# Kernel tuning notes

Hardware: AMD Instinct MI355X
Metric: run time of the kernel (lower is better)

Reference implementation:

```python
import jax, jax.numpy as jnp
import numpy as np

B, CD, E, H, K, L, NB = 262144, 2, 64, 128, 32, 6, 2
TB = 6.0
MIN_BIN = 1e-3      # nflows DEFAULT_MIN_BIN_WIDTH / HEIGHT
MIN_DERIV = 1e-3    # nflows DEFAULT_MIN_DERIVATIVE
P = 3 * K - 1       # spline params per feature


def _rq_spline(y, uw, uh, ud):
    """Unconstrained rational-quadratic spline (linear tails), forward pass.
    y: [B]; uw, uh: [B,K]; ud: [B,K-1]. Returns (z [B], logabsdet [B])."""
    inside = (y >= -TB) & (y <= TB)
    const = float(np.log(np.exp(1.0 - MIN_DERIV) - 1.0))
    ud = jnp.pad(ud, ((0, 0), (1, 1)), constant_values=const)  # boundary deriv -> 1
    w = jax.nn.softmax(uw, axis=-1)
    w = MIN_BIN + (1.0 - MIN_BIN * K) * w
    cw = jnp.pad(jnp.cumsum(w, -1), ((0, 0), (1, 0)))
    cw = (2.0 * TB) * cw - TB
    cw = cw.at[:, 0].set(-TB).at[:, -1].set(TB)
    w = cw[:, 1:] - cw[:, :-1]
    hgt = jax.nn.softmax(uh, axis=-1)
    hgt = MIN_BIN + (1.0 - MIN_BIN * K) * hgt
    ch = jnp.pad(jnp.cumsum(hgt, -1), ((0, 0), (1, 0)))
    ch = (2.0 * TB) * ch - TB
    ch = ch.at[:, 0].set(-TB).at[:, -1].set(TB)
    hgt = ch[:, 1:] - ch[:, :-1]
    d = MIN_DERIV + jax.nn.softplus(ud)                       # [B,K+1]
    yc = jnp.clip(y, -TB, TB)
    locs = cw.at[:, -1].add(1e-6)                             # nflows searchsorted eps
    idx = jnp.clip(jnp.sum((yc[:, None] >= locs).astype(jnp.int32), -1) - 1, 0, K - 1)
    g = lambda a, i: jnp.take_along_axis(a, i[:, None], axis=1)[:, 0]
    cw_k, w_k = g(cw, idx), g(w, idx)
    ch_k, h_k = g(ch, idx), g(hgt, idx)
    d_k, d_k1 = g(d, idx), g(d, idx + 1)
    s_k = h_k / w_k
    th = (yc - cw_k) / w_k
    th1m = th * (1.0 - th)
    num = h_k * (s_k * th * th + d_k * th1m)
    den = s_k + (d_k + d_k1 - 2.0 * s_k) * th1m
    out = ch_k + num / den
    dnum = s_k * s_k * (d_k1 * th * th + 2.0 * s_k * th1m + d_k * (1.0 - th) ** 2)
    lad = jnp.log(dnum) - 2.0 * jnp.log(den)
    return jnp.where(inside, out, y), jnp.where(inside, lad, 0.0)


def setup_inputs() -> dict:
    key = jax.random.key(0)
    ks = iter(jax.random.split(key, 32))
    w = lambda shape, fan: jax.random.normal(next(ks), shape, jnp.float32) / np.sqrt(fan)
    inp = {
        "y": jax.random.normal(next(ks), (B, 1), jnp.float32),
        "context": jax.random.normal(next(ks), (B, CD), jnp.float32),
        "eW1": w((CD, E), CD), "eb1": jnp.zeros((E,), jnp.float32),
        "eW2": w((E, E), E),   "eb2": jnp.zeros((E,), jnp.float32),
        "eW3": w((E, E), E),   "eb3": jnp.zeros((E,), jnp.float32),
        # per-layer MADE conditioner (input->hidden weight is masked to 0 for features=1)
        "init_b": w((L, H), 1.0),
        "ctx_W": w((L, E, H), E), "ctx_b": jnp.zeros((L, H), jnp.float32),
        "blk_W1": w((L, NB, H, H), H), "blk_b1": jnp.zeros((L, NB, H), jnp.float32),
        "blk_W2": w((L, NB, H, H), H), "blk_b2": jnp.zeros((L, NB, H), jnp.float32),
        "blk_Wc": w((L, NB, E, H), E), "blk_bc": jnp.zeros((L, NB, H), jnp.float32),
        "out_W": w((L, H, P), H), "out_b": jnp.zeros((L, P), jnp.float32),
    }
    return inp


def reference(y, context, eW1, eb1, eW2, eb2, eW3, eb3, init_b, ctx_W, ctx_b,
              blk_W1, blk_b1, blk_W2, blk_b2, blk_Wc, blk_bc, out_W, out_b):
    emb = jax.nn.elu(context @ eW1 + eb1)
    emb = jax.nn.elu(emb @ eW2 + eb2)
    emb = jax.nn.elu(emb @ eW3 + eb3)            # [B,E]
    z = y[:, 0]
    total_lad = jnp.zeros_like(z)
    scale = np.sqrt(H).astype(np.float32)        # nflows divides widths/heights by sqrt(hidden)
    for l in range(L):
        h = init_b[l] + emb @ ctx_W[l] + ctx_b[l]
        for j in range(NB):                       # masked residual blocks (fully open for features=1)
            t = jax.nn.elu(h) @ blk_W1[l, j] + blk_b1[l, j]
            t = jax.nn.elu(t) @ blk_W2[l, j] + blk_b2[l, j]
            gate = jax.nn.sigmoid(emb @ blk_Wc[l, j] + blk_bc[l, j])  # GLU with context
            h = h + t * gate
        p = h @ out_W[l] + out_b[l]               # [B, 3K-1]
        z, lad = _rq_spline(z, p[:, :K] / scale, p[:, K:2 * K] / scale, p[:, 2 * K:])
        total_lad = total_lad + lad
    log_prob = -0.5 * z * z - 0.5 * np.float32(np.log(2.0 * np.pi)) + total_lad
    return log_prob
```

## Files before the change

kernel.cpp:

```cpp
#include <hip/hip_runtime.h>
#include <math.h>

typedef _Float16 hfrag  __attribute__((ext_vector_type(8)));
typedef _Float16 hpack  __attribute__((ext_vector_type(4)));
typedef float    accf   __attribute__((ext_vector_type(16)));

constexpr float cTB = 6.0f;
constexpr float cMB = 0.001f;
constexpr float cMD = 0.001f;

constexpr int SH = 136;
constexpr int SE = 72;
constexpr int SP = 100;

__device__ __forceinline__ float eluf(float x)  { return x > 0.f ? x : __expf(x) - 1.f; }
__device__ __forceinline__ float sigmf(float x) { return 1.f / (1.f + __expf(-x)); }
__device__ __forceinline__ float softplusf_(float x) { return x > 20.f ? x : log1pf(__expf(x)); }

__global__ void prep_frag(const float* __restrict__ src, _Float16* __restrict__ dst,
                          int K, int F, int Fpad, int total) {
  int idx = blockIdx.x * 256 + threadIdx.x;
  if (idx >= total) return;
  const int j    = idx & 7;
  const int lane = (idx >> 3) & 63;
  const int rest = idx >> 9;
  const int csteps = K >> 4;
  const int cstep  = rest % csteps;
  const int rest2  = rest / csteps;
  const int fslices = Fpad >> 5;
  const int fs = rest2 % fslices;
  const int n  = rest2 / fslices;
  const int f  = fs * 32 + (lane & 31);
  const int k  = cstep * 16 + ((lane >> 5) << 3) + j;
  float v = (f < F) ? src[((size_t)n * K + k) * F + f] : 0.f;
  dst[idx] = (_Float16)v;
}

__global__ void prep_bias(const float* __restrict__ gib, const float* __restrict__ gcb,
                          const float* __restrict__ gob, float* __restrict__ cb,
                          float* __restrict__ ob) {
  int i = blockIdx.x * 256 + threadIdx.x;
  if (i < 768) cb[i] = gib[i] + gcb[i];
  if (i < 576) {
    int l = i / 96, f = i % 96;
    ob[i] = (f < 95) ? gob[l * 95 + f] : 0.f;
  }
}

#define GEMM2(WBASE, BPTR, BSTRIDE, KDIM, A0, A1)                              \
  _Pragma("unroll")                                                            \
  for (int c = 0; c < (KDIM); c += 16) {                                       \
    hfrag av = *(const hfrag*)((WBASE) + (c << 5) + lane8);                    \
    hfrag b0 = *(const hfrag*)((BPTR) + col * (BSTRIDE) + c + q8);             \
    hfrag b1 = *(const hfrag*)((BPTR) + (32 + col) * (BSTRIDE) + c + q8);      \
    A0 = __builtin_amdgcn_mfma_f32_32x32x16_f16(av, b0, A0, 0, 0, 0);          \
    A1 = __builtin_amdgcn_mfma_f32_32x32x16_f16(av, b1, A1, 0, 0, 0);          \
  }

__global__ __launch_bounds__(256, 4) void nsf_mfma(
    const float* __restrict__ gy,   const float* __restrict__ gctx,
    const float* __restrict__ eW1,  const float* __restrict__ eb1,
    const float* __restrict__ eb2,  const float* __restrict__ eb3,
    const float* __restrict__ cbias, const float* __restrict__ bb1,
    const float* __restrict__ bb2,  const float* __restrict__ bbc,
    const float* __restrict__ obias,
    const _Float16* __restrict__ wE2T, const _Float16* __restrict__ wE3T,
    const _Float16* __restrict__ wCtxT, const _Float16* __restrict__ wW1T,
    const _Float16* __restrict__ wW2T,  const _Float16* __restrict__ wWcT,
    const _Float16* __restrict__ wOutT, float* __restrict__ gout)
{
  __shared__ _Float16 sA[64 * SH];
  __shared__ _Float16 sE[64 * SE];
  __shared__ _Float16 sP[64 * SP];

  const int tid  = threadIdx.x;
  const int wid  = tid >> 6;
  const int lane = tid & 63;
  const int col  = lane & 31;
  const int q    = lane >> 5;
  const int q8   = q * 8;
  const int q4   = q * 4;
  const int f0   = wid * 32;
  const int m0   = blockIdx.x * 64;
  const int lane8 = lane * 8;

  {
    const int m  = tid & 63;
    const int eg = tid >> 6;
    const float2 c2 = *(const float2*)&gctx[(size_t)(m0 + m) * 2];
    #pragma unroll
    for (int j = 0; j < 16; ++j) {
      const int e = eg * 16 + j;
      sE[m * SE + e] = (_Float16)eluf(c2.x * eW1[e] + c2.y * eW1[64 + e] + eb1[e]);
    }
  }
  __syncthreads();
  {
    const int ft = wid & 1, nt = wid >> 1;
    accf a = {};
    const _Float16* wr = wE2T + ft * 2048;
    #pragma unroll
    for (int c = 0; c < 64; c += 16) {
      hfrag av = *(const hfrag*)(wr + (c << 5) + lane8);
      hfrag bv = *(const hfrag*)(&sE[(nt * 32 + col) * SE + c + q8]);
      a = __builtin_amdgcn_mfma_f32_32x32x16_f16(av, bv, a, 0, 0, 0);
    }
    const int mrow = nt * 32 + col;
    __syncthreads();
    #pragma unroll
    for (int g = 0; g < 4; ++g) {
      const int e = 32 * ft + 8 * g + q4;
      const float4 b = *(const float4*)&eb2[e];
      hpack pk;
      #pragma unroll
      for (int r = 0; r < 4; ++r) pk[r] = (_Float16)eluf(a[4 * g + r] + (&b.x)[r]);
      *(hpack*)&sA[mrow * SE + e] = pk;
    }
  }
  __syncthreads();
  {
    const int ft = wid & 1, nt = wid >> 1;
    accf a = {};
    const _Float16* wr = wE3T + ft * 2048;
    #pragma unroll
    for (int c = 0; c < 64; c += 16) {
      hfrag av = *(const hfrag*)(wr + (c << 5) + lane8);
      hfrag bv = *(const hfrag*)(&sA[(nt * 32 + col) * SE + c + q8]);
      a = __builtin_amdgcn_mfma_f32_32x32x16_f16(av, bv, a, 0, 0, 0);
    }
    const int mrow = nt * 32 + col;
    #pragma unroll
    for (int g = 0; g < 4; ++g) {
      const int e = 32 * ft + 8 * g + q4;
      const float4 b = *(const float4*)&eb3[e];
      hpack pk;
      #pragma unroll
      for (int r = 0; r < 4; ++r) pk[r] = (_Float16)eluf(a[4 * g + r] + (&b.x)[r]);
      *(hpack*)&sE[mrow * SE + e] = pk;
    }
  }
  __syncthreads();

  float z = 0.f, lad = 0.f;
  if (tid < 64) z = gy[m0 + tid];

  accf h0, h1;

  #pragma unroll 1
  for (int l = 0; l < 6; ++l) {
    {
      accf a0 = {}, a1 = {};
      const _Float16* wr = wCtxT + (size_t)l * 8192 + wid * 2048;
      GEMM2(wr, sE, SE, 64, a0, a1)
      #pragma unroll
      for (int nt = 0; nt < 2; ++nt) {
        accf& A = nt ? a1 : a0;
        accf& H = nt ? h1 : h0;
        const int mrow = nt * 32 + col;
        #pragma unroll
        for (int g = 0; g < 4; ++g) {
          const int f = f0 + 8 * g + q4;
          const float4 bi = *(const float4*)&cbias[l * 128 + f];
          hpack pk;
          #pragma unroll
          for (int r = 0; r < 4; ++r) {
            float hv = A[4 * g + r] + (&bi.x)[r];
            H[4 * g + r] = hv;
            pk[r] = (_Float16)eluf(hv);
          }
          *(hpack*)&sA[mrow * SH + f] = pk;
        }
      }
    }
    __syncthreads();

    #pragma unroll 1
    for (int jb = 0; jb < 2; ++jb) {
      const int wi = l * 2 + jb;
      {
        accf a0 = {}, a1 = {};
        const _Float16* wr = wW1T + (size_t)wi * 16384 + wid * 4096;
        GEMM2(wr, sA, SH, 128, a0, a1)
        __syncthreads();
        #pragma unroll
        for (int nt = 0; nt < 2; ++nt) {
          accf& A = nt ? a1 : a0;
          const int mrow = nt * 32 + col;
          #pragma unroll
          for (int g = 0; g < 4; ++g) {
            const int f = f0 + 8 * g + q4;
            const float4 bv = *(const float4*)&bb1[wi * 128 + f];
            hpack pk;
            #pragma unroll
            for (int r = 0; r < 4; ++r) pk[r] = (_Float16)eluf(A[4 * g + r] + (&bv.x)[r]);
            *(hpack*)&sA[mrow * SH + f] = pk;
          }
        }
      }
      __syncthreads();
      {
        hpack gpk[2][4];
        {
          accf g0 = {}, g1 = {};
          const _Float16* wrc = wWcT + (size_t)wi * 8192 + wid * 2048;
          GEMM2(wrc, sE, SE, 64, g0, g1)
          #pragma unroll
          for (int nt = 0; nt < 2; ++nt) {
            accf& AG = nt ? g1 : g0;
            #pragma unroll
            for (int g = 0; g < 4; ++g) {
              const int f = f0 + 8 * g + q4;
              const float4 bcv = *(const float4*)&bbc[wi * 128 + f];
              #pragma unroll
              for (int r = 0; r < 4; ++r)
                gpk[nt][g][r] = (_Float16)sigmf(AG[4 * g + r] + (&bcv.x)[r]);
            }
          }
        }
        __builtin_amdgcn_sched_barrier(0);
        accf a0 = {}, a1 = {};
        const _Float16* wr2 = wW2T + (size_t)wi * 16384 + wid * 4096;
        GEMM2(wr2, sA, SH, 128, a0, a1)
        __syncthreads();
        const bool last = (jb == 1);
        #pragma unroll
        for (int nt = 0; nt < 2; ++nt) {
          accf& A2 = nt ? a1 : a0;
          accf& H  = nt ? h1 : h0;
          const int mrow = nt * 32 + col;
          #pragma unroll
          for (int g = 0; g < 4; ++g) {
            const int f = f0 + 8 * g + q4;
            const float4 b2v = *(const float4*)&bb2[wi * 128 + f];
            hpack pk;
            #pragma unroll
            for (int r = 0; r < 4; ++r) {
              const float hv = H[4 * g + r] + (A2[4 * g + r] + (&b2v.x)[r]) * (float)gpk[nt][g][r];
              H[4 * g + r] = hv;
              pk[r] = (_Float16)(last ? hv : eluf(hv));
            }
            *(hpack*)&sA[mrow * SH + f] = pk;
          }
        }
      }
      __syncthreads();
    }

    if (wid < 3) {
      accf o0 = {}, o1 = {};
      const _Float16* wr = wOutT + (size_t)l * 12288 + wid * 4096;
      GEMM2(wr, sA, SH, 128, o0, o1)
      #pragma unroll
      for (int nt = 0; nt < 2; ++nt) {
        accf& A = nt ? o1 : o0;
        const int mrow = nt * 32 + col;
        #pragma unroll
        for (int g = 0; g < 4; ++g) {
          const int f = f0 + 8 * g + q4;
          const float4 ov = *(const float4*)&obias[l * 96 + f];
          hpack pk;
          #pragma unroll
          for (int r = 0; r < 4; ++r) pk[r] = (_Float16)(A[4 * g + r] + (&ov.x)[r]);
          *(hpack*)&sP[mrow * SP + f] = pk;
        }
      }
    }
    __syncthreads();

    if (tid < 64) {
      const float invS = 0.08838834764831845f;
      const _Float16* pmv = &sP[tid * SP];
      auto pm = [&](int i) -> float { return (float)pmv[i]; };
      float mw = pm(0), mh = pm(32);
      #pragma unroll
      for (int i = 1; i < 32; ++i) {
        mw = fmaxf(mw, pm(i));
        mh = fmaxf(mh, pm(32 + i));
      }
      float sw = 0.f, sh = 0.f;
      #pragma unroll
      for (int i = 0; i < 32; ++i) {
        sw += __expf((pm(i) - mw) * invS);
        sh += __expf((pm(32 + i) - mh) * invS);
      }
      const float cw_scale = (1.0f - cMB * 32.f) / sw;
      const float ch_scale = (1.0f - cMB * 32.f) / sh;
      const float yc = fminf(fmaxf(z, -cTB), cTB);

      int idx = 0;
      float cum = 0.f, cw_k = -cTB, cw_k1 = cTB;
      bool take = true;
      #pragma unroll
      for (int i = 1; i <= 32; ++i) {
        float cwi;
        if (i < 32) {
          cum += cMB + __expf((pm(i - 1) - mw) * invS) * cw_scale;
          cwi = 2.f * cTB * cum - cTB;
        } else {
          cwi = cTB;
        }
        if (take) { cw_k1 = cwi; take = false; }
        if (i < 32 && yc >= cwi) { idx = i; cw_k = cwi; take = true; }
      }

      cum = 0.f;
      float ch_k = -cTB, ch_k1 = cTB;
      #pragma unroll
      for (int i = 1; i < 32; ++i) {
        cum += cMB + __expf((pm(32 + i - 1) - mh) * invS) * ch_scale;
        const float chi = 2.f * cTB * cum - cTB;
        if (i == idx) ch_k = chi;
        if (i == idx + 1) ch_k1 = chi;
      }

      const float w_k = cw_k1 - cw_k;
      const float h_k = ch_k1 - ch_k;
      const float d_k  = (idx == 0)  ? 1.f : cMD + softplusf_(pm(64 + idx - 1));
      const float d_k1 = (idx == 31) ? 1.f : cMD + softplusf_(pm(64 + idx));

      const float s_k  = h_k / w_k;
      const float th   = (yc - cw_k) / w_k;
      const float th1m = th * (1.f - th);
      const float numv = h_k * (s_k * th * th + d_k * th1m);
      const float denv = s_k + (d_k + d_k1 - 2.f * s_k) * th1m;
      const float outv = ch_k + numv / denv;
      const float omt  = 1.f - th;
      const float dnum = s_k * s_k * (d_k1 * th * th + 2.f * s_k * th1m + d_k * omt * omt);
      const float ladv = __logf(dnum) - 2.f * __logf(denv);
      const bool inside = (z >= -cTB) && (z <= cTB);
      if (inside) { z = outv; lad += ladv; }
    }
  }

  if (tid < 64) {
    gout[m0 + tid] = -0.5f * z * z - 0.9189385332046727f + lad;
  }
}

extern "C" void kernel_launch(void* const* d_in, const int* in_sizes, int n_in,
                              void* d_out, int out_size, void* d_ws, size_t ws_size,
                              hipStream_t stream) {
  const float* gy   = (const float*)d_in[0];
  const float* gctx = (const float*)d_in[1];
  const float* eW1  = (const float*)d_in[2];
  const float* eb1  = (const float*)d_in[3];
  const float* eW2  = (const float*)d_in[4];
  const float* eb2  = (const float*)d_in[5];
  const float* eW3  = (const float*)d_in[6];
  const float* eb3  = (const float*)d_in[7];
  const float* gib  = (const float*)d_in[8];
  const float* gcW  = (const float*)d_in[9];
  const float* gcb  = (const float*)d_in[10];
  const float* bW1  = (const float*)d_in[11];
  const float* bb1  = (const float*)d_in[12];
  const float* bW2  = (const float*)d_in[13];
  const float* bb2  = (const float*)d_in[14];
  const float* bWc  = (const float*)d_in[15];
  const float* bbc  = (const float*)d_in[16];
  const float* goW  = (const float*)d_in[17];
  const float* gob  = (const float*)d_in[18];

  _Float16* ws    = (_Float16*)d_ws;
  _Float16* wE2T  = ws;
  _Float16* wE3T  = wE2T + 4096;
  _Float16* wCtxT = wE3T + 4096;
  _Float16* wW1T  = wCtxT + 49152;
  _Float16* wW2T  = wW1T + 196608;
  _Float16* wWcT  = wW2T + 196608;
  _Float16* wOutT = wWcT + 98304;
  float*    cb    = (float*)(wOutT + 73728);
  float*    ob    = cb + 768;

  auto prep = [&](const float* s, _Float16* d, int K, int F, int Fp, int n) {
    int tot = n * Fp * K;
    prep_frag<<<(tot + 255) / 256, 256, 0, stream>>>(s, d, K, F, Fp, tot);
  };
  prep(eW2, wE2T, 64, 64, 64, 1);
  prep(eW3, wE3T, 64, 64, 64, 1);
  prep(gcW, wCtxT, 64, 128, 128, 6);
  prep(bW1, wW1T, 128, 128, 128, 12);
  prep(bW2, wW2T, 128, 128, 128, 12);
  prep(bWc, wWcT, 64, 128, 128, 12);
  prep(goW, wOutT, 128, 95, 96, 6);
  prep_bias<<<3, 256, 0, stream>>>(gib, gcb, gob, cb, ob);

  nsf_mfma<<<dim3(262144 / 64), dim3(256), 0, stream>>>(
      gy, gctx, eW1, eb1, eb2, eb3, cb, bb1, bb2, bbc, ob,
      wE2T, wE3T, wCtxT, wW1T, wW2T, wWcT, wOutT, (float*)d_out);
}
```

Before: 850.6 us.

## Split each 64-row tile across 8 waves with one MFMA tile per wave

After: 995.9 us. 1.17x slower.

```diff
diff --git a/kernel.cpp b/kernel.cpp
--- a/kernel.cpp
+++ b/kernel.cpp
@@ -47,17 +47,15 @@
   }
 }
 
-#define GEMM2(WBASE, BPTR, BSTRIDE, KDIM, A0, A1)                              \
+#define GEMM1(WBASE, BPTR, BSTRIDE, KDIM, A0)                                  \
   _Pragma("unroll")                                                            \
   for (int c = 0; c < (KDIM); c += 16) {                                       \
     hfrag av = *(const hfrag*)((WBASE) + (c << 5) + lane8);                    \
-    hfrag b0 = *(const hfrag*)((BPTR) + col * (BSTRIDE) + c + q8);             \
-    hfrag b1 = *(const hfrag*)((BPTR) + (32 + col) * (BSTRIDE) + c + q8);      \
+    hfrag b0 = *(const hfrag*)((BPTR) + mrow * (BSTRIDE) + c + q8);            \
     A0 = __builtin_amdgcn_mfma_f32_32x32x16_f16(av, b0, A0, 0, 0, 0);          \
-    A1 = __builtin_amdgcn_mfma_f32_32x32x16_f16(av, b1, A1, 0, 0, 0);          \
-  }
-
-__global__ __launch_bounds__(256, 4) void nsf_mfma(
+  }
+
+__global__ __launch_bounds__(512, 8) void nsf_mfma(
     const float* __restrict__ gy,   const float* __restrict__ gctx,
     const float* __restrict__ eW1,  const float* __restrict__ eb1,
     const float* __restrict__ eb2,  const float* __restrict__ eb3,
@@ -80,7 +78,10 @@
   const int q    = lane >> 5;
   const int q8   = q * 8;
   const int q4   = q * 4;
-  const int f0   = wid * 32;
+  const int fs   = wid >> 1;
+  const int nt   = wid & 1;
+  const int f0   = fs * 32;
+  const int mrow = nt * 32 + col;
   const int m0   = blockIdx.x * 64;
   const int lane8 = lane * 8;
 
@@ -89,54 +90,60 @@
     const int eg = tid >> 6;
     const float2 c2 = *(const float2*)&gctx[(size_t)(m0 + m) * 2];
     #pragma unroll
-    for (int j = 0; j < 16; ++j) {
-      const int e = eg * 16 + j;
+    for (int j = 0; j < 8; ++j) {
+      const int e = eg * 8 + j;
       sE[m * SE + e] = (_Float16)eluf(c2.x * eW1[e] + c2.y * eW1[64 + e] + eb1[e]);
     }
   }
   __syncthreads();
   {
-    const int ft = wid & 1, nt = wid >> 1;
     accf a = {};
-    const _Float16* wr = wE2T + ft * 2048;
-    #pragma unroll
-    for (int c = 0; c < 64; c += 16) {
-      hfrag av = *(const hfrag*)(wr + (c << 5) + lane8);
-      hfrag bv = *(const hfrag*)(&sE[(nt * 32 + col) * SE + c + q8]);
-      a = __builtin_amdgcn_mfma_f32_32x32x16_f16(av, bv, a, 0, 0, 0);
-    }
-    const int mrow = nt * 32 + col;
+    const int ft = wid & 1, et = (wid >> 1) & 1;
+    if (wid < 4) {
+      const _Float16* wr = wE2T + ft * 2048;
+      #pragma unroll
+      for (int c = 0; c < 64; c += 16) {
+        hfrag av = *(const hfrag*)(wr + (c << 5) + lane8);
+        hfrag bv = *(const hfrag*)(&sE[(et * 32 + col) * SE + c + q8]);
+        a = __builtin_amdgcn_mfma_f32_32x32x16_f16(av, bv, a, 0, 0, 0);
+      }
+    }
     __syncthreads();
-    #pragma unroll
-    for (int g = 0; g < 4; ++g) {
-      const int e = 32 * ft + 8 * g + q4;
-      const float4 b = *(const float4*)&eb2[e];
-      hpack pk;
-      #pragma unroll
-      for (int r = 0; r < 4; ++r) pk[r] = (_Float16)eluf(a[4 * g + r] + (&b.x)[r]);
-      *(hpack*)&sA[mrow * SE + e] = pk;
+    if (wid < 4) {
+      const int erow = et * 32 + col;
+      #pragma unroll
+      for (int g = 0; g < 4; ++g) {
+        const int e = 32 * ft + 8 * g + q4;
+        const float4 b = *(const float4*)&eb2[e];
+        hpack pk;
+        #pragma unroll
+        for (int r = 0; r < 4; ++r) pk[r] = (_Float16)eluf(a[4 * g + r] + (&b.x)[r]);
+        *(hpack*)&sA[erow * SE + e] = pk;
+      }
     }
   }
   __syncthreads();
   {
-    const int ft = wid & 1, nt = wid >> 1;
-    accf a = {};
-    const _Float16* wr = wE3T + ft * 2048;
-    #pragma unroll
-    for (int c = 0; c < 64; c += 16) {
-      hfrag av = *(const hfrag*)(wr + (c << 5) + lane8);
-      hfrag bv = *(const hfrag*)(&sA[(nt * 32 + col) * SE + c + q8]);
-      a = __builtin_amdgcn_mfma_f32_32x32x16_f16(av, bv, a, 0, 0, 0);
-    }
-    const int mrow = nt * 32 + col;
-    #pragma unroll
-    for (int g = 0; g < 4; ++g) {
-      const int e = 32 * ft + 8 * g + q4;
-      const float4 b = *(const float4*)&eb3[e];
-      hpack pk;
-      #pragma unroll
-      for (int r = 0; r < 4; ++r) pk[r] = (_Float16)eluf(a[4 * g + r] + (&b.x)[r]);
-      *(hpack*)&sE[mrow * SE + e] = pk;
+    if (wid < 4) {
+      accf a = {};
+      const int ft = wid & 1, et = (wid >> 1) & 1;
+      const _Float16* wr = wE3T + ft * 2048;
+      #pragma unroll
+      for (int c = 0; c < 64; c += 16) {
+        hfrag av = *(const hfrag*)(wr + (c << 5) + lane8);
+        hfrag bv = *(const hfrag*)(&sA[(et * 32 + col) * SE + c + q8]);
+        a = __builtin_amdgcn_mfma_f32_32x32x16_f16(av, bv, a, 0, 0, 0);
+      }
+      const int erow = et * 32 + col;
+      #pragma unroll
+      for (int g = 0; g < 4; ++g) {
+        const int e = 32 * ft + 8 * g + q4;
+        const float4 b = *(const float4*)&eb3[e];
+        hpack pk;
+        #pragma unroll
+        for (int r = 0; r < 4; ++r) pk[r] = (_Float16)eluf(a[4 * g + r] + (&b.x)[r]);
+        *(hpack*)&sE[erow * SE + e] = pk;
+      }
     }
   }
   __syncthreads();
@@ -144,32 +151,26 @@
   float z = 0.f, lad = 0.f;
   if (tid < 64) z = gy[m0 + tid];
 
-  accf h0, h1;
+  accf h;
 
   #pragma unroll 1
   for (int l = 0; l < 6; ++l) {
     {
-      accf a0 = {}, a1 = {};
-      const _Float16* wr = wCtxT + (size_t)l * 8192 + wid * 2048;
-      GEMM2(wr, sE, SE, 64, a0, a1)
-      #pragma unroll
-      for (int nt = 0; nt < 2; ++nt) {
-        accf& A = nt ? a1 : a0;
-        accf& H = nt ? h1 : h0;
-        const int mrow = nt * 32 + col;
-        #pragma unroll
-        for (int g = 0; g < 4; ++g) {
-          const int f = f0 + 8 * g + q4;
-          const float4 bi = *(const float4*)&cbias[l * 128 + f];
-          hpack pk;
-          #pragma unroll
-          for (int r = 0; r < 4; ++r) {
-            float hv = A[4 * g + r] + (&bi.x)[r];
-            H[4 * g + r] = hv;
-            pk[r] = (_Float16)eluf(hv);
-          }
-          *(hpack*)&sA[mrow * SH + f] = pk;
-        }
+      accf a0 = {};
+      const _Float16* wr = wCtxT + (size_t)l * 8192 + fs * 2048;
+      GEMM1(wr, sE, SE, 64, a0)
+      #pragma unroll
+      for (int g = 0; g < 4; ++g) {
+        const int f = f0 + 8 * g + q4;
+        const float4 bi = *(const float4*)&cbias[l * 128 + f];
+        hpack pk;
+        #pragma unroll
+        for (int r = 0; r < 4; ++r) {
+          float hv = a0[4 * g + r] + (&bi.x)[r];
+          h[4 * g + r] = hv;
+          pk[r] = (_Float16)eluf(hv);
+        }
+        *(hpack*)&sA[mrow * SH + f] = pk;
       }
     }
     __syncthreads();
@@ -178,91 +179,71 @@
     for (int jb = 0; jb < 2; ++jb) {
       const int wi = l * 2 + jb;
       {
-        accf a0 = {}, a1 = {};
-        const _Float16* wr = wW1T + (size_t)wi * 16384 + wid * 4096;
-        GEMM2(wr, sA, SH, 128, a0, a1)
+        accf a0 = {};
+        const _Float16* wr = wW1T + (size_t)wi * 16384 + fs * 4096;
+        GEMM1(wr, sA, SH, 128, a0)
         __syncthreads();
         #pragma unroll
-        for (int nt = 0; nt < 2; ++nt) {
-          accf& A = nt ? a1 : a0;
-          const int mrow = nt * 32 + col;
+        for (int g = 0; g < 4; ++g) {
+          const int f = f0 + 8 * g + q4;
+          const float4 bv = *(const float4*)&bb1[wi * 128 + f];
+          hpack pk;
+          #pragma unroll
+          for (int r = 0; r < 4; ++r) pk[r] = (_Float16)eluf(a0[4 * g + r] + (&bv.x)[r]);
+          *(hpack*)&sA[mrow * SH + f] = pk;
+        }
+      }
+      __syncthreads();
+      {
+        hpack gpk[4];
+        {
+          accf g0 = {};
+          const _Float16* wrc = wWcT + (size_t)wi * 8192 + fs * 2048;
+          GEMM1(wrc, sE, SE, 64, g0)
           #pragma unroll
           for (int g = 0; g < 4; ++g) {
             const int f = f0 + 8 * g + q4;
-            const float4 bv = *(const float4*)&bb1[wi * 128 + f];
-            hpack pk;
+            const float4 bcv = *(const float4*)&bbc[wi * 128 + f];
             #pragma unroll
-            for (int r = 0; r < 4; ++r) pk[r] = (_Float16)eluf(A[4 * g + r] + (&bv.x)[r]);
-            *(hpack*)&sA[mrow * SH + f] = pk;
+            for (int r = 0; r < 4; ++r)
+              gpk[g][r] = (_Float16)sigmf(g0[4 * g + r] + (&bcv.x)[r]);
           }
         }
-      }
-      __syncthreads();
-      {
-        hpack gpk[2][4];
-        {
-          accf g0 = {}, g1 = {};
-          const _Float16* wrc = wWcT + (size_t)wi * 8192 + wid * 2048;
-          GEMM2(wrc, sE, SE, 64, g0, g1)
-          #pragma unroll
-          for (int nt = 0; nt < 2; ++nt) {
-            accf& AG = nt ? g1 : g0;
-            #pragma unroll
-            for (int g = 0; g < 4; ++g) {
-              const int f = f0 + 8 * g + q4;
-              const float4 bcv = *(const float4*)&bbc[wi * 128 + f];
-              #pragma unroll
-              for (int r = 0; r < 4; ++r)
-                gpk[nt][g][r] = (_Float16)sigmf(AG[4 * g + r] + (&bcv.x)[r]);
-            }
-          }
-        }
         __builtin_amdgcn_sched_barrier(0);
-        accf a0 = {}, a1 = {};
-        const _Float16* wr2 = wW2T + (size_t)wi * 16384 + wid * 4096;
-        GEMM2(wr2, sA, SH, 128, a0, a1)
+        accf a0 = {};
+        const _Float16* wr2 = wW2T + (size_t)wi * 16384 + fs * 4096;
+        GEMM1(wr2, sA, SH, 128, a0)
         __syncthreads();
         const bool last = (jb == 1);
         #pragma unroll
-        for (int nt = 0; nt < 2; ++nt) {
-          accf& A2 = nt ? a1 : a0;
-          accf& H  = nt ? h1 : h0;
-          const int mrow = nt * 32 + col;
-          #pragma unroll
-          for (int g = 0; g < 4; ++g) {
-            const int f = f0 + 8 * g + q4;
-            const float4 b2v = *(const float4*)&bb2[wi * 128 + f];
-            hpack pk;
-            #pragma unroll
-            for (int r = 0; r < 4; ++r) {
-              const float hv = H[4 * g + r] + (A2[4 * g + r] + (&b2v.x)[r]) * (float)gpk[nt][g][r];
-              H[4 * g + r] = hv;
-              pk[r] = (_Float16)(last ? hv : eluf(hv));
-            }
-            *(hpack*)&sA[mrow * SH + f] = pk;
-          }
-        }
-      }
-      __syncthreads();
-    }
-
-    if (wid < 3) {
-      accf o0 = {}, o1 = {};
-      const _Float16* wr = wOutT + (size_t)l * 12288 + wid * 4096;
-      GEMM2(wr, sA, SH, 128, o0, o1)
-      #pragma unroll
-      for (int nt = 0; nt < 2; ++nt) {
-        accf& A = nt ? o1 : o0;
-        const int mrow = nt * 32 + col;
-        #pragma unroll
         for (int g = 0; g < 4; ++g) {
           const int f = f0 + 8 * g + q4;
-          const float4 ov = *(const float4*)&obias[l * 96 + f];
+          const float4 b2v = *(const float4*)&bb2[wi * 128 + f];
           hpack pk;
           #pragma unroll
-          for (int r = 0; r < 4; ++r) pk[r] = (_Float16)(A[4 * g + r] + (&ov.x)[r]);
-          *(hpack*)&sP[mrow * SP + f] = pk;
-        }
+          for (int r = 0; r < 4; ++r) {
+            const float hv = h[4 * g + r] + (a0[4 * g + r] + (&b2v.x)[r]) * (float)gpk[g][r];
+            h[4 * g + r] = hv;
+            pk[r] = (_Float16)(last ? hv : eluf(hv));
+          }
+          *(hpack*)&sA[mrow * SH + f] = pk;
+        }
+      }
+      __syncthreads();
+    }
+
+    if (wid < 6) {
+      accf o0 = {};
+      const _Float16* wr = wOutT + (size_t)l * 12288 + fs * 4096;
+      GEMM1(wr, sA, SH, 128, o0)
+      #pragma unroll
+      for (int g = 0; g < 4; ++g) {
+        const int f = f0 + 8 * g + q4;
+        const float4 ov = *(const float4*)&obias[l * 96 + f];
+        hpack pk;
+        #pragma unroll
+        for (int r = 0; r < 4; ++r) pk[r] = (_Float16)(o0[4 * g + r] + (&ov.x)[r]);
+        *(hpack*)&sP[mrow * SP + f] = pk;
       }
     }
     __syncthreads();
@@ -384,7 +365,7 @@
   prep(goW, wOutT, 128, 95, 96, 6);
   prep_bias<<<3, 256, 0, stream>>>(gib, gcb, gob, cb, ob);
 
-  nsf_mfma<<<dim3(262144 / 64), dim3(256), 0, stream>>>(
+  nsf_mfma<<<dim3(262144 / 64), dim3(512), 0, stream>>>(
       gy, gctx, eW1, eb1, eb2, eb3, cb, bb1, bb2, bbc, ob,
       wE2T, wE3T, wCtxT, wW1T, wW2T, wWcT, wOutT, (float*)d_out);
 }
```
